# Optimization experiments

Measured on AMD Instinct MI355X. Metric: run time of the kernel, lower is better.

The kernel has to match this reference:

```python
import jax, jax.numpy as jnp
import numpy as np

B, S, HID = 1, 2048, 4096
NH, KVH, D = 32, 8, 128
MAXP = 2048
EPS = 1e-6


def _rope_tables(max_pos, dim, base=10000.0):
    inv_freq = 1.0 / (base ** (np.arange(0, dim, 2, dtype=np.float32) / dim))
    t = np.arange(max_pos, dtype=np.float32)
    freqs = np.outer(t, inv_freq)                      # [max_pos, dim/2]
    emb = np.concatenate([freqs, freqs], axis=-1)      # [max_pos, dim]
    return jnp.asarray(np.cos(emb)), jnp.asarray(np.sin(emb))


def setup_inputs() -> dict:
    key = jax.random.key(0)
    ks = jax.random.split(key, 6)
    x = jax.random.normal(ks[0], (B, S, HID), jnp.float32)
    scale = 0.02
    wq = jax.random.normal(ks[1], (NH * D, HID), jnp.float32) * scale
    wk = jax.random.normal(ks[2], (KVH * D, HID), jnp.float32) * scale
    wv = jax.random.normal(ks[3], (KVH * D, HID), jnp.float32) * scale
    wo = jax.random.normal(ks[4], (NH * D, HID), jnp.float32).T * scale  # stored as [HID, NH*D] -> transpose back
    wo = jnp.asarray(jax.random.normal(ks[4], (HID, NH * D), jnp.float32) * scale)
    cos_table, sin_table = _rope_tables(MAXP, D)
    return {
        "x": x, "wq": wq, "wk": wk, "wv": wv, "wo": wo,
        "q_norm_w": jnp.ones((D,), jnp.float32),
        "k_norm_w": jnp.ones((D,), jnp.float32),
        "cos_table": cos_table, "sin_table": sin_table,
        "k_cache": jnp.zeros((1, B, MAXP, KVH, D), jnp.float32),
        "v_cache": jnp.zeros((1, B, MAXP, KVH, D), jnp.float32),
        "positions": jnp.arange(S, dtype=jnp.int32),
        "layer_idx": 0,
    }


def _rmsnorm(x, w):
    return w * (x * jax.lax.rsqrt(jnp.mean(x * x, axis=-1, keepdims=True) + EPS))


def _rope(x, cos, sin):
    # x: [B, H, S, D]; cos/sin: [1, 1, S, D]
    half = x.shape[-1] // 2
    x1, x2 = x[..., :half], x[..., half:]
    rotated = jnp.concatenate([-x2, x1], axis=-1)
    return x * cos + rotated * sin


def reference(x, wq, wk, wv, wo, q_norm_w, k_norm_w, cos_table, sin_table,
              k_cache, v_cache, positions, layer_idx):
    bsz, seq_len, _ = x.shape
    d = q_norm_w.shape[0]
    nh = wq.shape[0] // d
    kvh = wk.shape[0] // d
    g = nh // kvh

    q = (x @ wq.T).reshape(bsz, seq_len, nh, d).transpose(0, 2, 1, 3)    # [B,NH,S,D]
    k = (x @ wk.T).reshape(bsz, seq_len, kvh, d).transpose(0, 2, 1, 3)   # [B,KVH,S,D]
    v = (x @ wv.T).reshape(bsz, seq_len, kvh, d).transpose(0, 2, 1, 3)

    q = _rmsnorm(q, q_norm_w)
    k = _rmsnorm(k, k_norm_w)

    cos = cos_table[positions][None, None]  # [1,1,S,D]
    sin = sin_table[positions][None, None]
    q = _rope(q, cos, sin)
    k = _rope(k, cos, sin)

    # KV-cache scatter at dynamic positions (prefill: positions = arange(S))
    kc = k_cache[layer_idx].at[:, positions].set(k.transpose(0, 2, 1, 3))
    vc = v_cache[layer_idx].at[:, positions].set(v.transpose(0, 2, 1, 3))
    # K = max(positions)+1 == seq_len in this (prefill) setup; static for jit
    K = seq_len
    k_all = kc[:, :K].transpose(0, 2, 1, 3)   # [B,KVH,K,D]
    v_all = vc[:, :K].transpose(0, 2, 1, 3)

    # GQA: group query heads instead of repeat_interleave on K/V (same math)
    qg = q.reshape(bsz, kvh, g, seq_len, d)
    scale = 1.0 / jnp.sqrt(jnp.asarray(d, q.dtype))
    scores = jnp.einsum('bkgqd,bkld->bkgql', qg, k_all) * scale
    causal = jnp.tril(jnp.ones((seq_len, K), dtype=bool))
    scores = jnp.where(causal, scores, jnp.finfo(scores.dtype).min)
    attn = jax.nn.softmax(scores, axis=-1)
    out = jnp.einsum('bkgql,bkld->bkgqd', attn, v_all)
    out = out.reshape(bsz, nh, seq_len, d).transpose(0, 2, 1, 3).reshape(bsz, seq_len, nh * d)
    return out @ wo.T
```

## Files before the change

### kernel.cpp

```cpp
#include <hip/hip_runtime.h>

typedef unsigned short u16;
typedef unsigned int u32;
typedef __attribute__((ext_vector_type(8))) short bf16x8;
typedef __attribute__((ext_vector_type(4))) float f32x4;
struct __align__(8) us4 { u16 x, y, z, w; };

#define S_LEN 2048
#define HID   4096
#define NH    32
#define KVH   8
#define HD    128

__device__ inline u16 f2bf(float f) {
  u32 u = __float_as_uint(f);
  u32 r = (u + 0x7fffu + ((u >> 16) & 1u)) >> 16;
  return (u16)r;
}
__device__ inline float bf2f(u16 h) { return __uint_as_float(((u32)h) << 16); }

__device__ inline void gld_lds16(const void* g, void* l) {
  __builtin_amdgcn_global_load_lds(
      (const __attribute__((address_space(1))) u32*)g,
      (__attribute__((address_space(3))) u32*)l, 16, 0, 0);
}

__global__ __launch_bounds__(256)
void cvt_all(const float* __restrict__ x, const float* __restrict__ wq,
             const float* __restrict__ wk, const float* __restrict__ wv,
             const float* __restrict__ wo, u16* __restrict__ xb,
             u16* __restrict__ wqb, u16* __restrict__ wkb,
             u16* __restrict__ wvb, u16* __restrict__ wob) {
  int b = blockIdx.x;
  const float* in; u16* out; int base;
  if (b < 8192)       { in = x;  out = xb;  base = b; }
  else if (b < 24576) { in = wq; out = wqb; base = b - 8192; }
  else if (b < 28672) { in = wk; out = wkb; base = b - 24576; }
  else if (b < 32768) { in = wv; out = wvb; base = b - 28672; }
  else                { in = wo; out = wob; base = b - 32768; }
  size_t i = ((size_t)base * 256 + threadIdx.x) * 4;
  f32x4 v = *(const f32x4*)(in + i);
  us4 o;
  o.x = f2bf(v[0]); o.y = f2bf(v[1]); o.z = f2bf(v[2]); o.w = f2bf(v[3]);
  *(us4*)(out + i) = o;
}

__device__ inline void gemm_core_128(const u16* __restrict__ A,
                                     const u16* __restrict__ W,
                                     int m0, int n0, int K,
                                     int kStart, int kEnd,
                                     u16* lA, u16* lB, f32x4 (&acc)[4][4]) {
  const int t = threadIdx.x;
  const int l = t & 63, w = t >> 6;
  const int quad = l >> 4, l15 = l & 15;
  const int wr = w >> 1, wc = w & 1;
  const int srow = t >> 2;
  const int scol = (t & 3) * 8;
#pragma unroll
  for (int i = 0; i < 4; i++)
#pragma unroll
    for (int j = 0; j < 4; j++) acc[i][j] = (f32x4){0.f, 0.f, 0.f, 0.f};

  for (int k0 = kStart; k0 < kEnd; k0 += 32) {
    gld_lds16(A + (size_t)(m0 + srow) * K + k0 + scol, lA + srow * 32 + scol);
    gld_lds16(A + (size_t)(m0 + 64 + srow) * K + k0 + scol, lA + (64 + srow) * 32 + scol);
    gld_lds16(W + (size_t)(n0 + srow) * K + k0 + scol, lB + srow * 32 + scol);
    gld_lds16(W + (size_t)(n0 + 64 + srow) * K + k0 + scol, lB + (64 + srow) * 32 + scol);
    __syncthreads();
    bf16x8 af[4], bfr[4];
#pragma unroll
    for (int i = 0; i < 4; i++)
      af[i] = *(const bf16x8*)(lA + (wr * 64 + i * 16 + l15) * 32 + quad * 8);
#pragma unroll
    for (int j = 0; j < 4; j++)
      bfr[j] = *(const bf16x8*)(lB + (wc * 64 + j * 16 + l15) * 32 + quad * 8);
#pragma unroll
    for (int i = 0; i < 4; i++)
#pragma unroll
      for (int j = 0; j < 4; j++)
        acc[i][j] = __builtin_amdgcn_mfma_f32_16x16x32_bf16(af[i], bfr[j], acc[i][j], 0, 0, 0);
    __syncthreads();
  }
}

#define QP_ELEMS (S_LEN * HID)
#define KP_ELEMS (S_LEN * 1024)
__global__ __launch_bounds__(256, 3)
void gemm_qkv(const u16* __restrict__ xb, const u16* __restrict__ wqb,
              const u16* __restrict__ wkb, const u16* __restrict__ wvb,
              u16* __restrict__ Qp0, u16* __restrict__ Kp0, u16* __restrict__ vt0) {
  __shared__ __align__(16) u16 lA[128 * 32];
  __shared__ __align__(16) u16 lB[128 * 32];
  const int bx = blockIdx.x;
  const int m0 = blockIdx.y * 128;
  const int z = blockIdx.z;
  const u16* W; u16* C; int n0, ldc, epi;
  if (bx < 32)      { W = wqb; C = Qp0 + (size_t)z * QP_ELEMS; n0 = bx * 128;        ldc = HID;  epi = 0; }
  else if (bx < 40) { W = wkb; C = Kp0 + (size_t)z * KP_ELEMS; n0 = (bx - 32) * 128; ldc = 1024; epi = 0; }
  else              { W = wvb; C = vt0 + (size_t)z * KP_ELEMS; n0 = (bx - 40) * 128; ldc = 0;    epi = 1; }

  f32x4 acc[4][4];
  gemm_core_128(xb, W, m0, n0, HID, z * 2048, z * 2048 + 2048, lA, lB, acc);

  const int t = threadIdx.x, l = t & 63, w = t >> 6;
  const int quad = l >> 4, l15 = l & 15;
  const int wr = w >> 1, wc = w & 1;
  if (epi == 0) {
#pragma unroll
    for (int i = 0; i < 4; i++) {
      int row0 = m0 + wr * 64 + i * 16 + quad * 4;
#pragma unroll
      for (int j = 0; j < 4; j++) {
        int col = n0 + wc * 64 + j * 16 + l15;
#pragma unroll
        for (int r = 0; r < 4; r++)
          C[(size_t)(row0 + r) * ldc + col] = f2bf(acc[i][j][r]);
      }
    }
  } else {
#pragma unroll
    for (int i = 0; i < 4; i++) {
      int row0 = m0 + wr * 64 + i * 16 + quad * 4;
#pragma unroll
      for (int j = 0; j < 4; j++) {
        int col = n0 + wc * 64 + j * 16 + l15;
        us4 v;
        v.x = f2bf(acc[i][j][0]); v.y = f2bf(acc[i][j][1]);
        v.z = f2bf(acc[i][j][2]); v.w = f2bf(acc[i][j][3]);
        *(us4*)(C + (size_t)col * S_LEN + row0) = v;
      }
    }
  }
}

__global__ __launch_bounds__(256, 3)
void gemm_out(const u16* __restrict__ ab, const u16* __restrict__ wob,
              float* __restrict__ O0, float* __restrict__ O1) {
  __shared__ __align__(16) u16 lA[128 * 32];
  __shared__ __align__(16) u16 lB[128 * 32];
  const int m0 = blockIdx.y * 128, n0 = blockIdx.x * 128;
  const int z = blockIdx.z;
  float* Op = z ? O1 : O0;
  f32x4 acc[4][4];
  gemm_core_128(ab, wob, m0, n0, HID, z * 2048, z * 2048 + 2048, lA, lB, acc);
  const int t = threadIdx.x, l = t & 63, w = t >> 6;
  const int quad = l >> 4, l15 = l & 15;
  const int wr = w >> 1, wc = w & 1;
#pragma unroll
  for (int i = 0; i < 4; i++) {
    int row0 = m0 + wr * 64 + i * 16 + quad * 4;
#pragma unroll
    for (int j = 0; j < 4; j++) {
      int col = n0 + wc * 64 + j * 16 + l15;
#pragma unroll
      for (int r = 0; r < 4; r++)
        Op[(size_t)(row0 + r) * HID + col] = acc[i][j][r];
    }
  }
}

__global__ __launch_bounds__(256)
void reduce_out(const float* __restrict__ O0, const float* __restrict__ O1,
                float* __restrict__ outp) {
  size_t i = ((size_t)blockIdx.x * 256 + threadIdx.x) * 4;
  f32x4 a = *(const f32x4*)(O0 + i);
  f32x4 b = *(const f32x4*)(O1 + i);
  a[0] += b[0]; a[1] += b[1]; a[2] += b[2]; a[3] += b[3];
  *(f32x4*)(outp + i) = a;
}

__global__ __launch_bounds__(256)
void rope_all(const u16* __restrict__ Qp0, const u16* __restrict__ Kp0,
              const float* __restrict__ qnw, const float* __restrict__ knw,
              const float* __restrict__ cosT, const float* __restrict__ sinT,
              const int* __restrict__ pos, u16* __restrict__ qbh,
              u16* __restrict__ kbh, const u16* __restrict__ vt0,
              u16* __restrict__ vt) {
  const int b = blockIdx.x;
  const int t = threadIdx.x, w = t >> 6, l = t & 63;
  if (b >= 20480) {
    size_t i = ((size_t)(b - 20480) * 256 + t) * 4;
    us4 a = *(const us4*)(vt0 + i);
    us4 c = *(const us4*)(vt0 + KP_ELEMS + i);
    us4 o;
    o.x = f2bf(bf2f(a.x) + bf2f(c.x)); o.y = f2bf(bf2f(a.y) + bf2f(c.y));
    o.z = f2bf(bf2f(a.z) + bf2f(c.z)); o.w = f2bf(bf2f(a.w) + bf2f(c.w));
    *(us4*)(vt + i) = o;
    return;
  }
  const u16 *xr0, *xr1; const float* nw; u16* orow; int s;
  if (b < 16384) {
    int p = b * 4 + w;
    s = p >> 5; int h = p & 31;
    xr0 = Qp0 + (size_t)s * HID + h * HD;
    xr1 = xr0 + QP_ELEMS;
    nw = qnw;
    orow = qbh + ((size_t)h * S_LEN + s) * HD;
  } else {
    int p = (b - 16384) * 4 + w;
    s = p >> 3; int h = p & 7;
    xr0 = Kp0 + (size_t)s * 1024 + h * HD;
    xr1 = xr0 + KP_ELEMS;
    nw = knw;
    orow = kbh + ((size_t)h * S_LEN + s) * HD;
  }
  float x1 = bf2f(xr0[l]) + bf2f(xr1[l]);
  float x2 = bf2f(xr0[l + 64]) + bf2f(xr1[l + 64]);
  float ss = x1 * x1 + x2 * x2;
#pragma unroll
  for (int m = 1; m < 64; m <<= 1) ss += __shfl_xor(ss, m);
  float rinv = rsqrtf(ss * (1.0f / 128.0f) + 1e-6f);
  float n1 = x1 * rinv * nw[l];
  float n2 = x2 * rinv * nw[l + 64];
  int ps = pos[s];
  float c1 = cosT[ps * HD + l], s1 = sinT[ps * HD + l];
  float c2 = cosT[ps * HD + l + 64], s2 = sinT[ps * HD + l + 64];
  float y1 = n1 * c1 - n2 * s1;
  float y2 = n2 * c2 + n1 * s2;
  orow[l] = f2bf(y1);
  orow[l + 64] = f2bf(y2);
}

__global__ __launch_bounds__(256)
void attn_fwd(const u16* __restrict__ qh, const u16* __restrict__ kbh,
              const u16* __restrict__ vth, u16* __restrict__ ab) {
  __shared__ __align__(16) u16 lK[64 * 128];
  __shared__ __align__(16) u16 lV[128 * 64];
  __shared__ __align__(16) u16 lP[4][16 * 72];
  const int t = threadIdx.x, w = t >> 6, l = t & 63;
  const int quad = l >> 4, l15 = l & 15;
  const int h = blockIdx.x;
  const int qt = 31 - blockIdx.y;
  const int kvh = h >> 2;
  const int q0 = qt * 64;
  const int qrow = q0 + w * 16 + l15;

  bf16x8 qf[4];
#pragma unroll
  for (int ks = 0; ks < 4; ks++)
    qf[ks] = *(const bf16x8*)(qh + ((size_t)h * S_LEN + qrow) * HD + ks * 32 + quad * 8);

  f32x4 accO[8];
#pragma unroll
  for (int j = 0; j < 8; j++) accO[j] = (f32x4){0.f, 0.f, 0.f, 0.f};
  float m_cur = -3.0e38f, l_sum = 0.f;
  const float scale = 0.08838834764831845f;

  const int ntiles = qt + 1;
  for (int tt = 0; tt < ntiles; tt++) {
    const int c0 = tt * 64;
#pragma unroll
    for (int i = 0; i < 4; i++) {
      int Cc = i * 256 + t;
      int r = Cc >> 4, ch = Cc & 15;
      int gch = ch ^ (r & 15);
      gld_lds16(kbh + ((size_t)kvh * S_LEN + c0 + r) * HD + gch * 8, lK + Cc * 8);
    }
#pragma unroll
    for (int i = 0; i < 4; i++) {
      int Cc = i * 256 + t;
      int d = Cc >> 3, ch = Cc & 7;
      int gch = ch ^ (d & 7);
      gld_lds16(vth + ((size_t)kvh * HD + d) * S_LEN + c0 + gch * 8, lV + Cc * 8);
    }
    __syncthreads();

    f32x4 st[4];
#pragma unroll
    for (int i = 0; i < 4; i++) {
      f32x4 sa = (f32x4){0.f, 0.f, 0.f, 0.f};
      int r = i * 16 + l15;
#pragma unroll
      for (int ks = 0; ks < 4; ks++) {
        int lc = ks * 4 + quad;
        bf16x8 kf = *(const bf16x8*)(lK + r * 128 + ((lc ^ (r & 15)) * 8));
        sa = __builtin_amdgcn_mfma_f32_16x16x32_bf16(kf, qf[ks], sa, 0, 0, 0);
      }
      st[i] = sa;
    }

    float tmax = -3.0e38f;
#pragma unroll
    for (int i = 0; i < 4; i++) {
#pragma unroll
      for (int r = 0; r < 4; r++) {
        int kcol = c0 + i * 16 + quad * 4 + r;
        float v = st[i][r] * scale;
        v = (kcol <= qrow) ? v : -3.0e38f;
        st[i][r] = v;
        tmax = fmaxf(tmax, v);
      }
    }
    tmax = fmaxf(tmax, __shfl_xor(tmax, 16));
    tmax = fmaxf(tmax, __shfl_xor(tmax, 32));
    float m_new = fmaxf(m_cur, tmax);
    float alpha = __expf(m_cur - m_new);

    float psum = 0.f;
#pragma unroll
    for (int i = 0; i < 4; i++) {
      us4 pv;
      u16* pp = (u16*)&pv;
#pragma unroll
      for (int r = 0; r < 4; r++) {
        float pe = __expf(st[i][r] - m_new);
        psum += pe;
        pp[r] = f2bf(pe);
      }
      *(us4*)(&lP[w][l15 * 72 + i * 16 + quad * 4]) = pv;
    }
    psum += __shfl_xor(psum, 16);
    psum += __shfl_xor(psum, 32);
    l_sum = l_sum * alpha + psum;
    m_cur = m_new;

#pragma unroll
    for (int r = 0; r < 4; r++) {
      float ar = __shfl(alpha, quad * 4 + r);
#pragma unroll
      for (int j = 0; j < 8; j++) accO[j][r] *= ar;
    }

    bf16x8 pf[2];
#pragma unroll
    for (int ks = 0; ks < 2; ks++)
      pf[ks] = *(const bf16x8*)(&lP[w][l15 * 72 + ks * 32 + quad * 8]);
#pragma unroll
    for (int j = 0; j < 8; j++) {
      int d = j * 16 + l15;
#pragma unroll
      for (int ks = 0; ks < 2; ks++) {
        int lc = ks * 4 + quad;
        bf16x8 vf = *(const bf16x8*)(lV + d * 64 + ((lc ^ (d & 7)) * 8));
        accO[j] = __builtin_amdgcn_mfma_f32_16x16x32_bf16(pf[ks], vf, accO[j], 0, 0, 0);
      }
    }
    __syncthreads();
  }

  float linv = 1.0f / l_sum;
#pragma unroll
  for (int r = 0; r < 4; r++) {
    float lr = __shfl(linv, quad * 4 + r);
    int row = q0 + w * 16 + quad * 4 + r;
#pragma unroll
    for (int j = 0; j < 8; j++) {
      int col = h * HD + j * 16 + l15;
      ab[(size_t)row * HID + col] = f2bf(accO[j][r] * lr);
    }
  }
}

extern "C" void kernel_launch(void* const* d_in, const int* in_sizes, int n_in,
                              void* d_out, int out_size, void* d_ws, size_t ws_size,
                              hipStream_t stream) {
  const float* x    = (const float*)d_in[0];
  const float* wq   = (const float*)d_in[1];
  const float* wk   = (const float*)d_in[2];
  const float* wv   = (const float*)d_in[3];
  const float* wo   = (const float*)d_in[4];
  const float* qnw  = (const float*)d_in[5];
  const float* knw  = (const float*)d_in[6];
  const float* cosT = (const float*)d_in[7];
  const float* sinT = (const float*)d_in[8];
  const int* positions = (const int*)d_in[11];

  char* ws = (char*)d_ws;
  u16* xb  = (u16*)(ws + 0ULL);
  u16* wqb = (u16*)(ws + 16777216ULL);
  u16* wkb = (u16*)(ws + 50331648ULL);
  u16* wvb = (u16*)(ws + 58720256ULL);
  u16* wob = (u16*)(ws + 67108864ULL);
  u16* Qp0 = (u16*)(ws + 100663296ULL);
  u16* Kp0 = (u16*)(ws + 134217728ULL);
  u16* vt0 = (u16*)(ws + 142606336ULL);
  u16* vt  = (u16*)(ws + 150994944ULL);
  u16* qbh = (u16*)(ws + 155189248ULL);
  u16* kbh = (u16*)(ws + 171966464ULL);
  u16* ab  = (u16*)(ws + 176160768ULL);
  float* O0 = (float*)(ws + 16777216ULL);
  float* O1 = (float*)(ws + 100663296ULL);

  cvt_all<<<49152, 256, 0, stream>>>(x, wq, wk, wv, wo, xb, wqb, wkb, wvb, wob);

  gemm_qkv<<<dim3(48, 16, 2), 256, 0, stream>>>(xb, wqb, wkb, wvb, Qp0, Kp0, vt0);

  rope_all<<<22528, 256, 0, stream>>>(Qp0, Kp0, qnw, knw, cosT, sinT, positions,
                                      qbh, kbh, vt0, vt);

  attn_fwd<<<dim3(NH, S_LEN / 64), 256, 0, stream>>>(qbh, kbh, vt, ab);

  gemm_out<<<dim3(HID / 128, S_LEN / 128, 2), 256, 0, stream>>>(ab, wob, O0, O1);
  reduce_out<<<8192, 256, 0, stream>>>(O0, O1, (float*)d_out);
}
```

Baseline: 541.2 us.

## Rebalance split-K across GEMMs, use bf16 partials, and streamline softmax masking

The QKV GEMM drops its two-way split-K and writes final bf16 results directly. This removes the partial buffers, the extra reads of them in rope_all, and the separate V-partial reduction. The output GEMM moves to a three-way split-K with bf16 partial outputs, summed in fp32 by reduce_out, which halves partial-write bytes but loses precision in the partials. In attention, the causal mask is applied only on diagonal tiles, and the softmax uses exp2 with log2(e) folded into the scale.

```diff
diff --git a/kernel.cpp b/kernel.cpp
--- a/kernel.cpp
+++ b/kernel.cpp
@@ -11,6 +11,7 @@
 #define NH    32
 #define KVH   8
 #define HD    128
+#define QP_ELEMS (S_LEN * HID)
 
 __device__ inline u16 f2bf(float f) {
   u32 u = __float_as_uint(f);
@@ -83,24 +84,21 @@
   }
 }
 
-#define QP_ELEMS (S_LEN * HID)
-#define KP_ELEMS (S_LEN * 1024)
 __global__ __launch_bounds__(256, 3)
 void gemm_qkv(const u16* __restrict__ xb, const u16* __restrict__ wqb,
               const u16* __restrict__ wkb, const u16* __restrict__ wvb,
-              u16* __restrict__ Qp0, u16* __restrict__ Kp0, u16* __restrict__ vt0) {
+              u16* __restrict__ Qp, u16* __restrict__ Kp, u16* __restrict__ vt) {
   __shared__ __align__(16) u16 lA[128 * 32];
   __shared__ __align__(16) u16 lB[128 * 32];
   const int bx = blockIdx.x;
   const int m0 = blockIdx.y * 128;
-  const int z = blockIdx.z;
   const u16* W; u16* C; int n0, ldc, epi;
-  if (bx < 32)      { W = wqb; C = Qp0 + (size_t)z * QP_ELEMS; n0 = bx * 128;        ldc = HID;  epi = 0; }
-  else if (bx < 40) { W = wkb; C = Kp0 + (size_t)z * KP_ELEMS; n0 = (bx - 32) * 128; ldc = 1024; epi = 0; }
-  else              { W = wvb; C = vt0 + (size_t)z * KP_ELEMS; n0 = (bx - 40) * 128; ldc = 0;    epi = 1; }
+  if (bx < 32)      { W = wqb; C = Qp; n0 = bx * 128;        ldc = HID;  epi = 0; }
+  else if (bx < 40) { W = wkb; C = Kp; n0 = (bx - 32) * 128; ldc = 1024; epi = 0; }
+  else              { W = wvb; C = vt; n0 = (bx - 40) * 128; ldc = 0;    epi = 1; }
 
   f32x4 acc[4][4];
-  gemm_core_128(xb, W, m0, n0, HID, z * 2048, z * 2048 + 2048, lA, lB, acc);
+  gemm_core_128(xb, W, m0, n0, HID, 0, HID, lA, lB, acc);
 
   const int t = threadIdx.x, l = t & 63, w = t >> 6;
   const int quad = l >> 4, l15 = l & 15;
@@ -135,14 +133,16 @@
 
 __global__ __launch_bounds__(256, 3)
 void gemm_out(const u16* __restrict__ ab, const u16* __restrict__ wob,
-              float* __restrict__ O0, float* __restrict__ O1) {
+              u16* __restrict__ Po) {
   __shared__ __align__(16) u16 lA[128 * 32];
   __shared__ __align__(16) u16 lB[128 * 32];
   const int m0 = blockIdx.y * 128, n0 = blockIdx.x * 128;
   const int z = blockIdx.z;
-  float* Op = z ? O1 : O0;
+  const int kStart = z * 1376;
+  const int kEnd = (z == 2) ? HID : kStart + 1376;
+  u16* C = Po + (size_t)z * QP_ELEMS;
   f32x4 acc[4][4];
-  gemm_core_128(ab, wob, m0, n0, HID, z * 2048, z * 2048 + 2048, lA, lB, acc);
+  gemm_core_128(ab, wob, m0, n0, HID, kStart, kEnd, lA, lB, acc);
   const int t = threadIdx.x, l = t & 63, w = t >> 6;
   const int quad = l >> 4, l15 = l & 15;
   const int wr = w >> 1, wc = w & 1;
@@ -154,58 +154,49 @@
       int col = n0 + wc * 64 + j * 16 + l15;
 #pragma unroll
       for (int r = 0; r < 4; r++)
-        Op[(size_t)(row0 + r) * HID + col] = acc[i][j][r];
+        C[(size_t)(row0 + r) * HID + col] = f2bf(acc[i][j][r]);
     }
   }
 }
 
 __global__ __launch_bounds__(256)
-void reduce_out(const float* __restrict__ O0, const float* __restrict__ O1,
-                float* __restrict__ outp) {
+void reduce_out(const u16* __restrict__ Po, float* __restrict__ outp) {
   size_t i = ((size_t)blockIdx.x * 256 + threadIdx.x) * 4;
-  f32x4 a = *(const f32x4*)(O0 + i);
-  f32x4 b = *(const f32x4*)(O1 + i);
-  a[0] += b[0]; a[1] += b[1]; a[2] += b[2]; a[3] += b[3];
-  *(f32x4*)(outp + i) = a;
+  us4 a = *(const us4*)(Po + i);
+  us4 b = *(const us4*)(Po + QP_ELEMS + i);
+  us4 c = *(const us4*)(Po + 2 * QP_ELEMS + i);
+  f32x4 o;
+  o[0] = bf2f(a.x) + bf2f(b.x) + bf2f(c.x);
+  o[1] = bf2f(a.y) + bf2f(b.y) + bf2f(c.y);
+  o[2] = bf2f(a.z) + bf2f(b.z) + bf2f(c.z);
+  o[3] = bf2f(a.w) + bf2f(b.w) + bf2f(c.w);
+  *(f32x4*)(outp + i) = o;
 }
 
 __global__ __launch_bounds__(256)
-void rope_all(const u16* __restrict__ Qp0, const u16* __restrict__ Kp0,
+void rope_all(const u16* __restrict__ Qp, const u16* __restrict__ Kp,
               const float* __restrict__ qnw, const float* __restrict__ knw,
               const float* __restrict__ cosT, const float* __restrict__ sinT,
               const int* __restrict__ pos, u16* __restrict__ qbh,
-              u16* __restrict__ kbh, const u16* __restrict__ vt0,
-              u16* __restrict__ vt) {
+              u16* __restrict__ kbh) {
   const int b = blockIdx.x;
   const int t = threadIdx.x, w = t >> 6, l = t & 63;
-  if (b >= 20480) {
-    size_t i = ((size_t)(b - 20480) * 256 + t) * 4;
-    us4 a = *(const us4*)(vt0 + i);
-    us4 c = *(const us4*)(vt0 + KP_ELEMS + i);
-    us4 o;
-    o.x = f2bf(bf2f(a.x) + bf2f(c.x)); o.y = f2bf(bf2f(a.y) + bf2f(c.y));
-    o.z = f2bf(bf2f(a.z) + bf2f(c.z)); o.w = f2bf(bf2f(a.w) + bf2f(c.w));
-    *(us4*)(vt + i) = o;
-    return;
-  }
-  const u16 *xr0, *xr1; const float* nw; u16* orow; int s;
+  const u16* xr; const float* nw; u16* orow; int s;
   if (b < 16384) {
     int p = b * 4 + w;
     s = p >> 5; int h = p & 31;
-    xr0 = Qp0 + (size_t)s * HID + h * HD;
-    xr1 = xr0 + QP_ELEMS;
+    xr = Qp + (size_t)s * HID + h * HD;
     nw = qnw;
     orow = qbh + ((size_t)h * S_LEN + s) * HD;
   } else {
     int p = (b - 16384) * 4 + w;
     s = p >> 3; int h = p & 7;
-    xr0 = Kp0 + (size_t)s * 1024 + h * HD;
-    xr1 = xr0 + KP_ELEMS;
+    xr = Kp + (size_t)s * 1024 + h * HD;
     nw = knw;
     orow = kbh + ((size_t)h * S_LEN + s) * HD;
   }
-  float x1 = bf2f(xr0[l]) + bf2f(xr1[l]);
-  float x2 = bf2f(xr0[l + 64]) + bf2f(xr1[l + 64]);
+  float x1 = bf2f(xr[l]);
+  float x2 = bf2f(xr[l + 64]);
   float ss = x1 * x1 + x2 * x2;
 #pragma unroll
   for (int m = 1; m < 64; m <<= 1) ss += __shfl_xor(ss, m);
@@ -244,7 +235,7 @@
 #pragma unroll
   for (int j = 0; j < 8; j++) accO[j] = (f32x4){0.f, 0.f, 0.f, 0.f};
   float m_cur = -3.0e38f, l_sum = 0.f;
-  const float scale = 0.08838834764831845f;
+  const float scale2 = 0.12751743f;
 
   const int ntiles = qt + 1;
   for (int tt = 0; tt < ntiles; tt++) {
@@ -279,22 +270,35 @@
       st[i] = sa;
     }
 
+    const bool needMask = (c0 + 63) > (q0 + w * 16);
     float tmax = -3.0e38f;
-#pragma unroll
-    for (int i = 0; i < 4; i++) {
-#pragma unroll
-      for (int r = 0; r < 4; r++) {
-        int kcol = c0 + i * 16 + quad * 4 + r;
-        float v = st[i][r] * scale;
-        v = (kcol <= qrow) ? v : -3.0e38f;
-        st[i][r] = v;
-        tmax = fmaxf(tmax, v);
+    if (needMask) {
+#pragma unroll
+      for (int i = 0; i < 4; i++) {
+#pragma unroll
+        for (int r = 0; r < 4; r++) {
+          int kcol = c0 + i * 16 + quad * 4 + r;
+          float v = st[i][r] * scale2;
+          v = (kcol <= qrow) ? v : -3.0e38f;
+          st[i][r] = v;
+          tmax = fmaxf(tmax, v);
+        }
+      }
+    } else {
+#pragma unroll
+      for (int i = 0; i < 4; i++) {
+#pragma unroll
+        for (int r = 0; r < 4; r++) {
+          float v = st[i][r] * scale2;
+          st[i][r] = v;
+          tmax = fmaxf(tmax, v);
+        }
       }
     }
     tmax = fmaxf(tmax, __shfl_xor(tmax, 16));
     tmax = fmaxf(tmax, __shfl_xor(tmax, 32));
     float m_new = fmaxf(m_cur, tmax);
-    float alpha = __expf(m_cur - m_new);
+    float alpha = exp2f(m_cur - m_new);
 
     float psum = 0.f;
 #pragma unroll
@@ -303,7 +307,7 @@
       u16* pp = (u16*)&pv;
 #pragma unroll
       for (int r = 0; r < 4; r++) {
-        float pe = __expf(st[i][r] - m_new);
+        float pe = exp2f(st[i][r] - m_new);
         psum += pe;
         pp[r] = f2bf(pe);
       }
@@ -366,30 +370,29 @@
   const int* positions = (const int*)d_in[11];
 
   char* ws = (char*)d_ws;
-  u16* xb  = (u16*)(ws + 0ULL);
-  u16* wqb = (u16*)(ws + 16777216ULL);
-  u16* wkb = (u16*)(ws + 50331648ULL);
-  u16* wvb = (u16*)(ws + 58720256ULL);
-  u16* wob = (u16*)(ws + 67108864ULL);
-  u16* Qp0 = (u16*)(ws + 100663296ULL);
-  u16* Kp0 = (u16*)(ws + 134217728ULL);
-  u16* vt0 = (u16*)(ws + 142606336ULL);
-  u16* vt  = (u16*)(ws + 150994944ULL);
-  u16* qbh = (u16*)(ws + 155189248ULL);
-  u16* kbh = (u16*)(ws + 171966464ULL);
-  u16* ab  = (u16*)(ws + 176160768ULL);
-  float* O0 = (float*)(ws + 16777216ULL);
-  float* O1 = (float*)(ws + 100663296ULL);
+  const size_t MB = 1048576ULL;
+  u16* xb  = (u16*)(ws + 0 * MB);
+  u16* wqb = (u16*)(ws + 16 * MB);
+  u16* wkb = (u16*)(ws + 48 * MB);
+  u16* wvb = (u16*)(ws + 56 * MB);
+  u16* wob = (u16*)(ws + 64 * MB);
+  u16* Qp  = (u16*)(ws + 96 * MB);
+  u16* Kp  = (u16*)(ws + 112 * MB);
+  u16* vt  = (u16*)(ws + 116 * MB);
+  u16* qbh = (u16*)(ws + 120 * MB);
+  u16* kbh = (u16*)(ws + 136 * MB);
+  u16* ab  = (u16*)(ws + 140 * MB);
+  u16* Po  = (u16*)(ws + 0 * MB);
 
   cvt_all<<<49152, 256, 0, stream>>>(x, wq, wk, wv, wo, xb, wqb, wkb, wvb, wob);
 
-  gemm_qkv<<<dim3(48, 16, 2), 256, 0, stream>>>(xb, wqb, wkb, wvb, Qp0, Kp0, vt0);
-
-  rope_all<<<22528, 256, 0, stream>>>(Qp0, Kp0, qnw, knw, cosT, sinT, positions,
-                                      qbh, kbh, vt0, vt);
+  gemm_qkv<<<dim3(48, 16), 256, 0, stream>>>(xb, wqb, wkb, wvb, Qp, Kp, vt);
+
+  rope_all<<<20480, 256, 0, stream>>>(Qp, Kp, qnw, knw, cosT, sinT, positions,
+                                      qbh, kbh);
 
   attn_fwd<<<dim3(NH, S_LEN / 64), 256, 0, stream>>>(qbh, kbh, vt, ab);
 
-  gemm_out<<<dim3(HID / 128, S_LEN / 128, 2), 256, 0, stream>>>(ab, wob, O0, O1);
-  reduce_out<<<8192, 256, 0, stream>>>(O0, O1, (float*)d_out);
-}
+  gemm_out<<<dim3(HID / 128, S_LEN / 128, 3), 256, 0, stream>>>(ab, wob, Po);
+  reduce_out<<<8192, 256, 0, stream>>>(Po, (float*)d_out);
+}
```

After: 541.8 us. Within noise of the previous version (+0.1%).
